# Performance work log

Hardware: AMD Instinct MI355X
Metric: run time of the kernel (lower is better)

The kernel has to match this reference:

```python
import jax, jax.numpy as jnp
import numpy as np

CHUNK = 256
ROPE_BASE = 10000.0
EPS = 1e-6


def setup_inputs() -> dict:
    key = jax.random.key(0)
    ks = jax.random.split(key, 8)
    B, N, D, H, K = 4, 8192, 1024, 16, 4
    x = jax.random.normal(ks[0], (B, N, D), dtype=jnp.float32)
    norm_scale = jnp.ones((D,), dtype=jnp.float32)
    conv_w = jax.random.normal(ks[1], (D, 1, K), dtype=jnp.float32) * 0.2
    conv_b = jax.random.normal(ks[2], (D,), dtype=jnp.float32) * 0.02
    in_proj_w = jax.random.normal(ks[3], (D, 3 * D), dtype=jnp.float32) * 0.02
    dt_bias = jax.random.normal(ks[4], (D,), dtype=jnp.float32) * 0.5
    head_mix = jnp.eye(H, dtype=jnp.float32) + 0.02 * jax.random.normal(ks[5], (H, H), dtype=jnp.float32)
    out_proj_w = jax.random.normal(ks[6], (D, D), dtype=jnp.float32) * 0.02
    return {"x": x, "norm_scale": norm_scale, "conv_w": conv_w, "conv_b": conv_b,
            "in_proj_w": in_proj_w, "dt_bias": dt_bias, "head_mix": head_mix,
            "out_proj_w": out_proj_w}


def _rmsnorm(x, scale):
    xf = x.astype(jnp.float32)
    rms = jax.lax.rsqrt(jnp.mean(xf * xf, axis=-1, keepdims=True) + EPS)
    out = scale.astype(jnp.float32) * (xf * rms)
    return jnp.clip(out, -60000.0, 60000.0).astype(x.dtype)


def _rope(v, N, d_head, dtype):
    # v: (B, N, H, d_head); cos/sin: (N, d_head//2)
    half = d_head // 2
    inv_freq = 1.0 / (ROPE_BASE ** (jnp.arange(0, d_head, 2, dtype=jnp.float32) / d_head))
    freqs = jnp.arange(N, dtype=jnp.float32)[:, None] * inv_freq[None, :]
    cos = jnp.cos(freqs).astype(dtype)[None, :, None, :]
    sin = jnp.sin(freqs).astype(dtype)[None, :, None, :]
    v1, v2 = v[..., :half], v[..., half:]
    return jnp.concatenate([v1 * cos - v2 * sin, v1 * sin + v2 * cos], axis=-1)


def reference(x, norm_scale, conv_w, conv_b, in_proj_w, dt_bias, head_mix, out_proj_w):
    residual = x
    B, N, D = x.shape
    H = head_mix.shape[0]
    d_head = D // H
    xn = _rmsnorm(x, norm_scale)

    # depthwise causal conv: torch pads K-1 both sides then truncates to N -> left-pad only
    K = conv_w.shape[-1]
    xc = jax.lax.conv_general_dilated(
        xn.transpose(0, 2, 1), conv_w, window_strides=(1,), padding=[(K - 1, 0)],
        feature_group_count=D, dimension_numbers=("NCH", "OIH", "NCH"))
    xc = (xc + conv_b[None, :, None]).transpose(0, 2, 1)  # (B, N, D)
    xc = xc * jax.nn.sigmoid(xc)  # SiLU

    fused = xc @ in_proj_w  # (B, N, 3D)
    dt_raw, v, gate_raw = jnp.split(fused, 3, axis=-1)
    dt = jnp.clip(jax.nn.softplus(dt_raw.astype(jnp.float32) + dt_bias.astype(jnp.float32)),
                  0.001, 2.0).astype(dt_raw.dtype)
    gate = jax.nn.sigmoid(gate_raw)
    log_alpha = -dt.astype(jnp.float32)

    v_rot = _rope(v.reshape(B, N, H, d_head), N, d_head, x.dtype).reshape(B, N, D)
    v_in = (v_rot * dt).astype(jnp.float32)

    # pad to multiple of CHUNK (static)
    pad = (-N) % CHUNK
    if pad:
        v_in = jnp.pad(v_in, ((0, 0), (0, pad), (0, 0)))
        log_alpha = jnp.pad(log_alpha, ((0, 0), (0, pad), (0, 0)))
    Np = N + pad
    nc = Np // CHUNK
    v_ch = v_in.reshape(B, nc, CHUNK, D)
    la_ch = log_alpha.reshape(B, nc, CHUNK, D)

    # intra-chunk stabilized cumulative scan
    L = jnp.clip(jnp.cumsum(la_ch, axis=2), -20.0, 0.0)
    L_max = jnp.max(L, axis=2, keepdims=True)
    L_st = L - L_max
    cum_scaled = jnp.cumsum(jnp.exp(-L_st) * v_ch, axis=2)
    chunk_out = jnp.exp(L_st) * cum_scaled  # (B, nc, CHUNK, D)

    if nc > 1:
        # inter-chunk carry, fully parallel
        bdecay = L[:, :, -1, :]            # (B, nc, D)
        bout = chunk_out[:, :, -1, :]      # (B, nc, D)
        cum_decay = jnp.clip(jnp.cumsum(bdecay, axis=1), -80.0, 0.0)
        stab = jnp.max(cum_decay, axis=1, keepdims=True)
        ncd = jnp.clip(cum_decay - stab, -20.0, 0.0)
        seeds = bout * jnp.exp(-ncd)
        shifted = jnp.pad(seeds[:, :-1], ((0, 0), (1, 0), (0, 0)))
        carries = jnp.cumsum(shifted, axis=1) * jnp.exp(ncd)  # (B, nc, D)
        final = chunk_out + carries[:, :, None, :] * jnp.exp(L)
    else:
        final = chunk_out
    final = final.astype(x.dtype).reshape(B, Np, D)[:, :N, :]

    v_mix = jnp.einsum("bnhd,hm->bnmd", final.reshape(B, N, H, d_head), head_mix)
    final = v_mix.reshape(B, N, D)
    out = (final * gate) @ out_proj_w
    return residual + out
```

## Files before the change

### kernel.cpp

```cpp
#include <hip/hip_runtime.h>

#define TOK 32768
#define DMODEL 1024
#define NSEQ 8192
#define NCHK 32
#define CHUNKC 256
#define KDIM 1024
#define NKT (KDIM / 64)
#define LOG2E 1.44269504f

typedef __attribute__((ext_vector_type(8))) short bf16x8;
typedef __attribute__((ext_vector_type(4))) float f32x4;

__device__ __forceinline__ unsigned short f2bf(float f) {
  unsigned u = __float_as_uint(f);
  u += 0x7fffu + ((u >> 16) & 1u);
  return (unsigned short)(u >> 16);
}
__device__ __forceinline__ float bf2f(unsigned short h) {
  return __uint_as_float(((unsigned)h) << 16);
}
__device__ __forceinline__ float sigm(float x) {
  return __builtin_amdgcn_rcpf(1.f + exp2f(-LOG2E * x));
}

typedef __attribute__((address_space(3))) unsigned int lds_u32_t;
typedef const __attribute__((address_space(1))) unsigned int glb_u32_t;

__device__ __forceinline__ void gl_lds16(const void* g, void* l) {
  __builtin_amdgcn_global_load_lds((glb_u32_t*)g, (lds_u32_t*)l, 16, 0, 0);
}

__global__ __launch_bounds__(256) void transpose_bf16_k(const float* __restrict__ in,
                                                        unsigned short* __restrict__ out,
                                                        int R, int C) {
  __shared__ float tile[32][33];
  const int c0 = blockIdx.x * 32, r0 = blockIdx.y * 32;
  const int tx = threadIdx.x, ty = threadIdx.y;
#pragma unroll
  for (int i = 0; i < 32; i += 8)
    tile[ty + i][tx] = in[(long)(r0 + ty + i) * C + c0 + tx];
  __syncthreads();
#pragma unroll
  for (int i = 0; i < 32; i += 8)
    out[(long)(c0 + ty + i) * R + r0 + tx] = f2bf(tile[tx][ty + i]);
}

__global__ __launch_bounds__(256) void ropetab_k(float2* __restrict__ tab) {
  const int i = blockIdx.x * 256 + threadIdx.x;
  const int f = i & 31, n = i >> 5;
  const float invf = exp2f(-(float)f * (13.287712379549449f / 32.0f));
  const float ang = (float)n * invf;
  tab[i] = make_float2(cosf(ang), sinf(ang));
}

__global__ __launch_bounds__(256) void rmsconv_k(const float* __restrict__ x,
                                                 const float* __restrict__ scale,
                                                 const float* __restrict__ w,
                                                 const float* __restrict__ cb,
                                                 unsigned short* __restrict__ xc) {
  __shared__ float xs[11][1024];
  __shared__ float red[4];
  const int t = threadIdx.x;
  const long row0 = (long)blockIdx.x * 8;
  const bool seqstart = ((row0 & (NSEQ - 1)) == 0);
  const float4 sc = ((const float4*)scale)[t];
  for (int i = 0; i < 11; ++i) {
    if (i < 3 && seqstart) {
      ((float4*)xs[i])[t] = make_float4(0.f, 0.f, 0.f, 0.f);
      continue;
    }
    const long r = row0 - 3 + i;
    const float4 v = ((const float4*)(x + r * DMODEL))[t];
    float ss = v.x * v.x + v.y * v.y + v.z * v.z + v.w * v.w;
#pragma unroll
    for (int off = 32; off > 0; off >>= 1) ss += __shfl_down(ss, off);
    if ((t & 63) == 0) red[t >> 6] = ss;
    __syncthreads();
    const float tot = red[0] + red[1] + red[2] + red[3];
    const float rr = rsqrtf(tot * (1.0f / DMODEL) + 1e-6f);
    float4 o;
    o.x = fminf(fmaxf(v.x * rr * sc.x, -60000.f), 60000.f);
    o.y = fminf(fmaxf(v.y * rr * sc.y, -60000.f), 60000.f);
    o.z = fminf(fmaxf(v.z * rr * sc.z, -60000.f), 60000.f);
    o.w = fminf(fmaxf(v.w * rr * sc.w, -60000.f), 60000.f);
    ((float4*)xs[i])[t] = o;
    __syncthreads();
  }
  __syncthreads();
  const int d0 = t * 4;
  float wl[4][4];
#pragma unroll
  for (int j = 0; j < 4; ++j) {
    const float4 t4 = *(const float4*)(w + (d0 + j) * 4);
    wl[j][0] = t4.x; wl[j][1] = t4.y; wl[j][2] = t4.z; wl[j][3] = t4.w;
  }
  const float4 cb4 = ((const float4*)cb)[t];
#pragma unroll
  for (int orow = 0; orow < 8; ++orow) {
    float o[4] = {0.f, 0.f, 0.f, 0.f};
#pragma unroll
    for (int k = 0; k < 4; ++k) {
      const float4 xv = ((const float4*)xs[orow + k])[t];
      o[0] += xv.x * wl[0][k]; o[1] += xv.y * wl[1][k];
      o[2] += xv.z * wl[2][k]; o[3] += xv.w * wl[3][k];
    }
    ushort4 st;
    { const float a = o[0] + cb4.x; st.x = f2bf(a * sigm(a)); }
    { const float a = o[1] + cb4.y; st.y = f2bf(a * sigm(a)); }
    { const float a = o[2] + cb4.z; st.z = f2bf(a * sigm(a)); }
    { const float a = o[3] + cb4.w; st.w = f2bf(a * sigm(a)); }
    *(ushort4*)(xc + (row0 + orow) * DMODEL + d0) = st;
  }
}

template <int EPI>
__global__ __launch_bounds__(256) void gemm_bt(const unsigned short* __restrict__ A,
                                               const unsigned short* __restrict__ BT,
                                               unsigned short* dtb, unsigned short* vrotb,
                                               unsigned short* gateb,
                                               const float* __restrict__ dt_bias,
                                               const float2* __restrict__ tab,
                                               float* outp, const float* __restrict__ resid) {
  __shared__ unsigned short As[2][128 * 64];
  __shared__ unsigned short Bs[2][128 * 64];
  const int tid = threadIdx.x;
  const int l = tid & 63;
  const int w = tid >> 6;
  const int wr = w >> 1, wc = w & 1;

  constexpr int NBN = (EPI == 0) ? 24 : 8;
  constexpr int XB = 32;
  const int lin = blockIdx.y * NBN + blockIdx.x;
  const int xcd = lin & 7;
  const int g = lin >> 3;
  const int band = g / (NBN * 8);
  const int j = g - band * (NBN * 8);
  const int bmoff = j / NBN;
  const int bn = j - bmoff * NBN;
  const int bm = xcd * XB + band * 8 + bmoff;

  f32x4 acc[4][4];
#pragma unroll
  for (int m = 0; m < 4; ++m)
#pragma unroll
    for (int n = 0; n < 4; ++n) acc[m][n] = {0.f, 0.f, 0.f, 0.f};

  const int lr = l >> 3;
  const int lc = ((l & 7) ^ lr) * 8;
  const unsigned short* aG[4];
  const unsigned short* bG[4];
  int chofs[4];
#pragma unroll
  for (int i = 0; i < 4; ++i) {
    const int ch = w + i * 4;
    aG[i] = A + ((long)(bm * 128 + ch * 8 + lr)) * KDIM + lc;
    bG[i] = BT + ((long)(bn * 128 + ch * 8 + lr)) * KDIM + lc;
    chofs[i] = ch * 512;
  }

  const int sw = (l & 7) * 8;
  const int col0 = ((l >> 4) * 8) ^ sw;
  const int col1 = (32 + (l >> 4) * 8) ^ sw;

#define STAGE(buf, k0)                              \
  {                                                 \
    _Pragma("unroll")                               \
    for (int i = 0; i < 4; ++i) {                   \
      gl_lds16(aG[i] + (k0), &As[buf][chofs[i]]);   \
      gl_lds16(bG[i] + (k0), &Bs[buf][chofs[i]]);   \
    }                                               \
  }

  auto compute = [&](int cur) {
    const unsigned short* Ab = &As[cur][0];
    const unsigned short* Bb = &Bs[cur][0];
#pragma unroll
    for (int kk = 0; kk < 2; ++kk) {
      const int ck = kk ? col1 : col0;
      bf16x8 af[4], bfr[4];
#pragma unroll
      for (int m = 0; m < 4; ++m)
        af[m] = *(const bf16x8*)&Ab[(wr * 64 + m * 16 + (l & 15)) * 64 + ck];
#pragma unroll
      for (int n = 0; n < 4; ++n)
        bfr[n] = *(const bf16x8*)&Bb[(wc * 64 + n * 16 + (l & 15)) * 64 + ck];
#pragma unroll
      for (int m = 0; m < 4; ++m)
#pragma unroll
        for (int n = 0; n < 4; ++n)
          acc[m][n] = __builtin_amdgcn_mfma_f32_16x16x32_bf16(af[m], bfr[n], acc[m][n], 0, 0, 0);
    }
  };

  STAGE(0, 0);
  __syncthreads();
  int cur = 0;
  for (int kt = 0; kt < NKT - 1; ++kt) {
    STAGE(cur ^ 1, (kt + 1) * 64);
    compute(cur);
    __syncthreads();
    cur ^= 1;
  }
  compute(cur);
#undef STAGE

  const int rbase = bm * 128 + wr * 64;
  const int cbase = bn * 128 + wc * 64;
  const int lr4 = (l >> 4) * 4;
  const int lc16 = l & 15;

  if constexpr (EPI == 0) {
    const int seg = cbase >> 10;
    if (seg == 0) {
#pragma unroll
      for (int m = 0; m < 4; ++m)
#pragma unroll
        for (int n = 0; n < 4; ++n) {
          const int c = (cbase & 1023) + n * 16 + lc16;
          const float bias = dt_bias[c];
#pragma unroll
          for (int j2 = 0; j2 < 4; ++j2) {
            const int row = rbase + m * 16 + lr4 + j2;
            const float a = acc[m][n][j2] + bias;
            const float e2 = exp2f(-LOG2E * fabsf(a));
            const float sp = fmaxf(a, 0.f) + 0.69314718f * log2f(1.f + e2);
            dtb[(long)row * DMODEL + c] = f2bf(fminf(fmaxf(sp, 0.001f), 2.0f));
          }
        }
    } else if (seg == 1) {
#pragma unroll
      for (int m = 0; m < 4; ++m)
#pragma unroll
        for (int n = 0; n < 2; ++n) {
          const int dd = n * 16 + lc16;
          const int c = (cbase & 1023) + dd;
#pragma unroll
          for (int j2 = 0; j2 < 4; ++j2) {
            const int row = rbase + m * 16 + lr4 + j2;
            const int pos = row & (NSEQ - 1);
            const float2 cs = tab[pos * 32 + dd];
            const float v1 = acc[m][n][j2], v2 = acc[m][n + 2][j2];
            vrotb[(long)row * DMODEL + c]      = f2bf(v1 * cs.x - v2 * cs.y);
            vrotb[(long)row * DMODEL + c + 32] = f2bf(v1 * cs.y + v2 * cs.x);
          }
        }
    } else {
#pragma unroll
      for (int m = 0; m < 4; ++m)
#pragma unroll
        for (int n = 0; n < 4; ++n) {
          const int c = (cbase & 1023) + n * 16 + lc16;
#pragma unroll
          for (int j2 = 0; j2 < 4; ++j2) {
            const int row = rbase + m * 16 + lr4 + j2;
            gateb[(long)row * DMODEL + c] = f2bf(sigm(acc[m][n][j2]));
          }
        }
    }
  } else {
#pragma unroll
    for (int m = 0; m < 4; ++m)
#pragma unroll
      for (int n = 0; n < 4; ++n) {
        const int col = cbase + n * 16 + lc16;
#pragma unroll
        for (int j2 = 0; j2 < 4; ++j2) {
          const int row = rbase + m * 16 + lr4 + j2;
          const long o = (long)row * DMODEL + col;
          outp[o] = resid[o] + acc[m][n][j2];
        }
      }
  }
}

__global__ __launch_bounds__(256) void scan1_k(const unsigned short* __restrict__ dt,
                                               const unsigned short* __restrict__ vrotb,
                                               float* __restrict__ Llast,
                                               float* __restrict__ bout) {
  const int idx = blockIdx.x * 256 + threadIdx.x;
  const int d = idx & 1023;
  const int ch = (idx >> 10) & 31;
  const int b = idx >> 15;
  const long base = ((long)b * NSEQ + ch * CHUNKC) * DMODEL + d;
  float run = 0.f, s = 0.f, L = 0.f;
#pragma unroll 4
  for (int c = 0; c < CHUNKC; ++c) {
    const float dtv = bf2f(dt[base + (long)c * DMODEL]);
    const float vv = bf2f(vrotb[base + (long)c * DMODEL]) * dtv;
    run -= dtv;
    L = fminf(fmaxf(run, -20.f), 0.f);
    s += exp2f(-LOG2E * L) * vv;
  }
  Llast[idx] = L;
  bout[idx] = exp2f(LOG2E * L) * s;
}

__global__ __launch_bounds__(256) void scan2_k(const float* __restrict__ Llast,
                                               const float* __restrict__ bout,
                                               float* __restrict__ carry) {
  const int idx = blockIdx.x * 256 + threadIdx.x;
  const int d = idx & 1023;
  const int b = idx >> 10;
  const long base = (long)b * (NCHK * DMODEL) + d;
  float cd[NCHK];
  float run = 0.f, stab = -1e30f;
#pragma unroll
  for (int ch = 0; ch < NCHK; ++ch) {
    run += Llast[base + ch * DMODEL];
    cd[ch] = fminf(fmaxf(run, -80.f), 0.f);
    stab = fmaxf(stab, cd[ch]);
  }
  float acc = 0.f;
#pragma unroll
  for (int ch = 0; ch < NCHK; ++ch) {
    const float ncd = fminf(fmaxf(cd[ch] - stab, -20.f), 0.f);
    carry[base + ch * DMODEL] = acc * exp2f(LOG2E * ncd);
    acc += bout[base + ch * DMODEL] * exp2f(-LOG2E * ncd);
  }
}

__global__ __launch_bounds__(256) void scan3_k(const unsigned short* __restrict__ dt,
                                               unsigned short* vrotb,
                                               const float* __restrict__ carry) {
  const int idx = blockIdx.x * 256 + threadIdx.x;
  const int d = idx & 1023;
  const int ch = (idx >> 10) & 31;
  const int b = idx >> 15;
  const long base = ((long)b * NSEQ + ch * CHUNKC) * DMODEL + d;
  const float ce = carry[idx];
  float run = 0.f, s = 0.f;
#pragma unroll 4
  for (int c = 0; c < CHUNKC; ++c) {
    const long o = base + (long)c * DMODEL;
    const float dtv = bf2f(dt[o]);
    const float vv = bf2f(vrotb[o]) * dtv;
    run -= dtv;
    const float L = fminf(fmaxf(run, -20.f), 0.f);
    s += exp2f(-LOG2E * L) * vv;
    vrotb[o] = f2bf(exp2f(LOG2E * L) * (s + ce));
  }
}

__global__ __launch_bounds__(256) void headmix_k(const unsigned short* __restrict__ fin,
                                                 const unsigned short* __restrict__ gateb,
                                                 const float* __restrict__ hm,
                                                 unsigned short* __restrict__ A2) {
  __shared__ float mixs[256];
  const int t = threadIdx.x;
  mixs[t] = hm[t];
  __syncthreads();
  const long row = (long)blockIdx.x * 4 + (t >> 6);
  const int dd = t & 63;
  const unsigned short* f = fin + row * DMODEL + dd;
  float fv[16];
#pragma unroll
  for (int h = 0; h < 16; ++h) fv[h] = bf2f(f[h * 64]);
#pragma unroll
  for (int m = 0; m < 16; ++m) {
    float o = 0.f;
#pragma unroll
    for (int h = 0; h < 16; ++h) o += fv[h] * mixs[h * 16 + m];
    const long c = row * DMODEL + m * 64 + dd;
    A2[c] = f2bf(o * bf2f(gateb[c]));
  }
}

extern "C" void kernel_launch(void* const* d_in, const int* in_sizes, int n_in,
                              void* d_out, int out_size, void* d_ws, size_t ws_size,
                              hipStream_t stream) {
  const float* x        = (const float*)d_in[0];
  const float* nscale   = (const float*)d_in[1];
  const float* conv_w   = (const float*)d_in[2];
  const float* conv_b   = (const float*)d_in[3];
  const float* in_proj  = (const float*)d_in[4];
  const float* dt_bias  = (const float*)d_in[5];
  const float* head_mix = (const float*)d_in[6];
  const float* out_proj = (const float*)d_in[7];
  float* out = (float*)d_out;

  char* p = (char*)d_ws;
  unsigned short* W1T = (unsigned short*)p; p += (size_t)3072 * 1024 * 2;
  unsigned short* W2T = (unsigned short*)p; p += (size_t)1024 * 1024 * 2;
  float2* tab  = (float2*)p; p += (size_t)NSEQ * 32 * sizeof(float2);
  float* Llast = (float*)p;  p += (size_t)131072 * 4;
  float* bout  = (float*)p;  p += (size_t)131072 * 4;
  float* carry = (float*)p;  p += (size_t)131072 * 4;
  unsigned short* dtb   = (unsigned short*)p; p += (size_t)TOK * DMODEL * 2;
  unsigned short* xc    = (unsigned short*)p; p += (size_t)TOK * DMODEL * 2;
  unsigned short* vrotb = (unsigned short*)p; p += (size_t)TOK * DMODEL * 2;
  unsigned short* gateb = (unsigned short*)p; p += (size_t)TOK * DMODEL * 2;

  transpose_bf16_k<<<dim3(96, 32), dim3(32, 8), 0, stream>>>(in_proj, W1T, 1024, 3072);
  transpose_bf16_k<<<dim3(32, 32), dim3(32, 8), 0, stream>>>(out_proj, W2T, 1024, 1024);
  ropetab_k<<<1024, 256, 0, stream>>>(tab);
  rmsconv_k<<<TOK / 8, 256, 0, stream>>>(x, nscale, conv_w, conv_b, xc);

  gemm_bt<0><<<dim3(24, 256), 256, 0, stream>>>(xc, W1T, dtb, vrotb, gateb,
                                                dt_bias, tab, nullptr, nullptr);
  scan1_k<<<512, 256, 0, stream>>>(dtb, vrotb, Llast, bout);
  scan2_k<<<16, 256, 0, stream>>>(Llast, bout, carry);
  scan3_k<<<512, 256, 0, stream>>>(dtb, vrotb, carry);
  headmix_k<<<TOK / 4, 256, 0, stream>>>(vrotb, gateb, head_mix, xc );
  gemm_bt<1><<<dim3(8, 256), 256, 0, stream>>>(xc, W2T, nullptr, nullptr, nullptr,
                                               nullptr, nullptr, out, x);
}
```

Measured before the change: 700.9 us.

## Switch GEMM to triple-buffered BK=32 pipeline with XCD-aware supertile swizzle

The bf16 GEMM kernels move from a 2-stage BK=64 double buffer to a 3-stage BK=32 ring buffer. Loads are kept two tiles ahead, with explicit vmcnt waits and raw barriers in place of __syncthreads. LDS swizzle and global load addressing are redone for the narrower tile, MFMA sections are wrapped in s_setprio, and block-to-tile mapping now groups 4xSBN supertiles per XCD for L2 reuse. The aim is to hide global-load latency better and improve cache locality, at the cost of twice as many barriers per K step and more complex wait-count logic.

```diff
diff --git a/kernel.cpp b/kernel.cpp
--- a/kernel.cpp
+++ b/kernel.cpp
@@ -6,7 +6,7 @@
 #define NCHK 32
 #define CHUNKC 256
 #define KDIM 1024
-#define NKT (KDIM / 64)
+#define NKT (KDIM / 32)
 #define LOG2E 1.44269504f
 
 typedef __attribute__((ext_vector_type(8))) short bf16x8;
@@ -114,7 +114,7 @@
   }
 }
 
-template <int EPI>
+template <int EPI, int NBN, int SBN>
 __global__ __launch_bounds__(256) void gemm_bt(const unsigned short* __restrict__ A,
                                                const unsigned short* __restrict__ BT,
                                                unsigned short* dtb, unsigned short* vrotb,
@@ -122,23 +122,26 @@
                                                const float* __restrict__ dt_bias,
                                                const float2* __restrict__ tab,
                                                float* outp, const float* __restrict__ resid) {
-  __shared__ unsigned short As[2][128 * 64];
-  __shared__ unsigned short Bs[2][128 * 64];
+  __shared__ unsigned short As[3][128 * 32];
+  __shared__ unsigned short Bs[3][128 * 32];
   const int tid = threadIdx.x;
   const int l = tid & 63;
   const int w = tid >> 6;
   const int wr = w >> 1, wc = w & 1;
 
-  constexpr int NBN = (EPI == 0) ? 24 : 8;
-  constexpr int XB = 32;
+  constexpr int BPS = 4 * SBN;
+  constexpr int NBNS = NBN / SBN;
   const int lin = blockIdx.y * NBN + blockIdx.x;
   const int xcd = lin & 7;
   const int g = lin >> 3;
-  const int band = g / (NBN * 8);
-  const int j = g - band * (NBN * 8);
-  const int bmoff = j / NBN;
-  const int bn = j - bmoff * NBN;
-  const int bm = xcd * XB + band * 8 + bmoff;
+  const int s = g / BPS;
+  const int r = g - s * BPS;
+  const int bmo = r / SBN;
+  const int bno = r - bmo * SBN;
+  const int bmS = s / NBNS;
+  const int bnS = s - bmS * NBNS;
+  const int bm = xcd * 32 + bmS * 4 + bmo;
+  const int bn = bnS * SBN + bno;
 
   f32x4 acc[4][4];
 #pragma unroll
@@ -146,62 +149,60 @@
 #pragma unroll
     for (int n = 0; n < 4; ++n) acc[m][n] = {0.f, 0.f, 0.f, 0.f};
 
-  const int lr = l >> 3;
-  const int lc = ((l & 7) ^ lr) * 8;
-  const unsigned short* aG[4];
-  const unsigned short* bG[4];
-  int chofs[4];
-#pragma unroll
-  for (int i = 0; i < 4; ++i) {
-    const int ch = w + i * 4;
-    aG[i] = A + ((long)(bm * 128 + ch * 8 + lr)) * KDIM + lc;
-    bG[i] = BT + ((long)(bn * 128 + ch * 8 + lr)) * KDIM + lc;
-    chofs[i] = ch * 512;
-  }
-
-  const int sw = (l & 7) * 8;
-  const int col0 = ((l >> 4) * 8) ^ sw;
-  const int col1 = (32 + (l >> 4) * 8) ^ sw;
-
-#define STAGE(buf, k0)                              \
-  {                                                 \
-    _Pragma("unroll")                               \
-    for (int i = 0; i < 4; ++i) {                   \
-      gl_lds16(aG[i] + (k0), &As[buf][chofs[i]]);   \
-      gl_lds16(bG[i] + (k0), &Bs[buf][chofs[i]]);   \
-    }                                               \
-  }
+  const int srcc = (((l & 3) ^ ((l >> 3) & 3)) * 8);
+  const unsigned short* aGb = A + ((long)(bm * 128 + w * 16 + (l >> 2))) * KDIM + srcc;
+  const unsigned short* bGb = BT + ((long)(bn * 128 + w * 16 + (l >> 2))) * KDIM + srcc;
+  const int ldso = (w * 16) * 32;
+
+#define STAGE(buf, k0)                                          \
+  {                                                             \
+    gl_lds16(aGb + (k0),               &As[buf][ldso]);         \
+    gl_lds16(aGb + (k0) + 64 * KDIM,   &As[buf][ldso + 2048]);  \
+    gl_lds16(bGb + (k0),               &Bs[buf][ldso]);         \
+    gl_lds16(bGb + (k0) + 64 * KDIM,   &Bs[buf][ldso + 2048]);  \
+  }
+
+  const int eoff = (((l >> 4) ^ ((l >> 1) & 3)) * 8);
+  const int arow = (wr * 64 + (l & 15)) * 32 + eoff;
+  const int brow = (wc * 64 + (l & 15)) * 32 + eoff;
 
   auto compute = [&](int cur) {
     const unsigned short* Ab = &As[cur][0];
     const unsigned short* Bb = &Bs[cur][0];
-#pragma unroll
-    for (int kk = 0; kk < 2; ++kk) {
-      const int ck = kk ? col1 : col0;
-      bf16x8 af[4], bfr[4];
-#pragma unroll
-      for (int m = 0; m < 4; ++m)
-        af[m] = *(const bf16x8*)&Ab[(wr * 64 + m * 16 + (l & 15)) * 64 + ck];
+    bf16x8 af[4], bfr[4];
+#pragma unroll
+    for (int m = 0; m < 4; ++m) af[m] = *(const bf16x8*)&Ab[arow + m * 512];
+#pragma unroll
+    for (int n = 0; n < 4; ++n) bfr[n] = *(const bf16x8*)&Bb[brow + n * 512];
+    __builtin_amdgcn_s_setprio(1);
+#pragma unroll
+    for (int m = 0; m < 4; ++m)
 #pragma unroll
       for (int n = 0; n < 4; ++n)
-        bfr[n] = *(const bf16x8*)&Bb[(wc * 64 + n * 16 + (l & 15)) * 64 + ck];
-#pragma unroll
-      for (int m = 0; m < 4; ++m)
-#pragma unroll
-        for (int n = 0; n < 4; ++n)
-          acc[m][n] = __builtin_amdgcn_mfma_f32_16x16x32_bf16(af[m], bfr[n], acc[m][n], 0, 0, 0);
-    }
+        acc[m][n] = __builtin_amdgcn_mfma_f32_16x16x32_bf16(af[m], bfr[n], acc[m][n], 0, 0, 0);
+    __builtin_amdgcn_s_setprio(0);
   };
 
   STAGE(0, 0);
-  __syncthreads();
-  int cur = 0;
-  for (int kt = 0; kt < NKT - 1; ++kt) {
-    STAGE(cur ^ 1, (kt + 1) * 64);
+  STAGE(1, 32);
+  int cur = 0, nxt = 2;
+  for (int t = 0; t < NKT - 2; ++t) {
+    __builtin_amdgcn_s_barrier();
+    STAGE(nxt, (t + 2) * 32);
+    asm volatile("s_waitcnt vmcnt(8)" ::: "memory");
+    __builtin_amdgcn_s_barrier();
     compute(cur);
-    __syncthreads();
-    cur ^= 1;
-  }
+    cur = (cur == 2) ? 0 : cur + 1;
+    nxt = (nxt == 2) ? 0 : nxt + 1;
+  }
+  __builtin_amdgcn_s_barrier();
+  asm volatile("s_waitcnt vmcnt(4)" ::: "memory");
+  __builtin_amdgcn_s_barrier();
+  compute(cur);
+  cur = (cur == 2) ? 0 : cur + 1;
+  __builtin_amdgcn_s_barrier();
+  asm volatile("s_waitcnt vmcnt(0)" ::: "memory");
+  __builtin_amdgcn_s_barrier();
   compute(cur);
 #undef STAGE
 
@@ -396,12 +397,12 @@
   ropetab_k<<<1024, 256, 0, stream>>>(tab);
   rmsconv_k<<<TOK / 8, 256, 0, stream>>>(x, nscale, conv_w, conv_b, xc);
 
-  gemm_bt<0><<<dim3(24, 256), 256, 0, stream>>>(xc, W1T, dtb, vrotb, gateb,
-                                                dt_bias, tab, nullptr, nullptr);
+  gemm_bt<0, 24, 6><<<dim3(24, 256), 256, 0, stream>>>(xc, W1T, dtb, vrotb, gateb,
+                                                       dt_bias, tab, nullptr, nullptr);
   scan1_k<<<512, 256, 0, stream>>>(dtb, vrotb, Llast, bout);
   scan2_k<<<16, 256, 0, stream>>>(Llast, bout, carry);
   scan3_k<<<512, 256, 0, stream>>>(dtb, vrotb, carry);
   headmix_k<<<TOK / 4, 256, 0, stream>>>(vrotb, gateb, head_mix, xc );
-  gemm_bt<1><<<dim3(8, 256), 256, 0, stream>>>(xc, W2T, nullptr, nullptr, nullptr,
-                                               nullptr, nullptr, out, x);
-}
+  gemm_bt<1, 8, 8><<<dim3(8, 256), 256, 0, stream>>>(xc, W2T, nullptr, nullptr, nullptr,
+                                                     nullptr, nullptr, out, x);
+}
```

Result: slower. 723.2 us (+3.2%).
